# Performance work log

Hardware: AMD Instinct MI355X
Metric: run time of the kernel (lower is better)

The kernel has to match this reference:

```python
import jax, jax.numpy as jnp
import numpy as np

NUM_HEADS = 16

def setup_inputs() -> dict:
    key = jax.random.key(0)
    k1, k2, k3 = jax.random.split(key, 3)
    B, N, C = 2, 2048, 1024
    x = jax.random.normal(k1, (B, N, C), dtype=jnp.float32)
    w_qkv = jax.random.normal(k2, (C, 3 * C), dtype=jnp.float32) * (C ** -0.5)
    w_proj = jax.random.normal(k3, (C, C), dtype=jnp.float32) * (C ** -0.5)
    b_proj = jnp.zeros((C,), dtype=jnp.float32)
    return {"x": x, "w_qkv": w_qkv, "w_proj": w_proj, "b_proj": b_proj}

def reference(x, w_qkv, w_proj, b_proj):
    B, N, C = x.shape
    H = NUM_HEADS
    D = C // H
    scale = D ** -0.5
    qkv = (x @ w_qkv).reshape(B, N, 3, H, D).transpose(2, 0, 3, 1, 4)  # [3,B,H,N,D]
    q, k, v = qkv[0], qkv[1], qkv[2]
    attn = jnp.einsum("bhnd,bhmd->bhnm", q, k) * scale  # [B,H,N,N]
    attn = jax.nn.softmax(attn, axis=-1)
    out = jnp.einsum("bhnm,bhmd->bhnd", attn, v)  # [B,H,N,D]
    out = out.transpose(0, 2, 1, 3).reshape(B, N, C)
    return out @ w_proj + b_proj
```

## Files before the change

kernel.cpp:

```cpp
#include <hip/hip_runtime.h>
#include <hip/hip_bf16.h>
#include <math.h>

#define B_SZ   2
#define N_SEQ  2048
#define C_DIM  1024
#define H_NUM  16
#define D_HEAD 64
#define M_ROWS (B_SZ * N_SEQ)
#define QKV_N  (3 * C_DIM)

typedef __attribute__((ext_vector_type(8))) short  bf16x8;
typedef __attribute__((ext_vector_type(4))) float  floatx4;

static __device__ __forceinline__ unsigned short f2bf(float x) {
    unsigned int u = __float_as_uint(x);
    u = (u + 0x7FFFu + ((u >> 16) & 1u)) >> 16;
    return (unsigned short)u;
}
static __device__ __forceinline__ unsigned int f2bf_hi(float x) {
    unsigned int u = __float_as_uint(x);
    return u + 0x7FFFu + ((u >> 16) & 1u);
}
#if __has_builtin(__builtin_amdgcn_cvt_pk_bf16_f32)
typedef __bf16 bf16_2 __attribute__((ext_vector_type(2)));
static __device__ __forceinline__ unsigned int pkbf(float a, float b) {
    union { bf16_2 v; unsigned int u; } c;
    c.v = __builtin_amdgcn_cvt_pk_bf16_f32(a, b);
    return c.u;
}
#else
static __device__ __forceinline__ unsigned int pkbf(float a, float b) {
    return __builtin_amdgcn_perm(f2bf_hi(b), f2bf_hi(a), 0x07060302u);
}
#endif

#if __has_builtin(__builtin_amdgcn_exp2f)
#define EXP2F(x) __builtin_amdgcn_exp2f(x)
#else
#define EXP2F(x) exp2f(x)
#endif

#define GLP(p) ((const __attribute__((address_space(1))) void*)(p))
#define LDP(p) ((__attribute__((address_space(3))) void*)(p))

#define CEXP 0.18033688011112042f

__global__ __launch_bounds__(256)
void prep_fused(const float* __restrict__ x,      unsigned short* __restrict__ xb,
                const float* __restrict__ w_qkv,  unsigned short* __restrict__ wqkvT,
                const float* __restrict__ w_proj, unsigned short* __restrict__ wprojT)
{
    __shared__ unsigned short t[64][72];
    const int bid = blockIdx.x;
    const int tid = threadIdx.x;

    if (bid < 4096) {
        const int i = bid * 256 + tid;
        float4 v = ((const float4*)x)[i];
        ushort4 p;
        p.x = f2bf(v.x); p.y = f2bf(v.y); p.z = f2bf(v.z); p.w = f2bf(v.w);
        ((ushort4*)xb)[i] = p;
        return;
    }

    const float* W;
    unsigned short* WT;
    int N, tt;
    if (bid < 4096 + 768) { W = w_qkv;  WT = wqkvT;  N = QKV_N; tt = bid - 4096; }
    else                  { W = w_proj; WT = wprojT; N = C_DIM; tt = bid - 4864; }
    const int ntiles = N / 64;
    const int n0 = (tt % ntiles) * 64;
    const int k0 = (tt / ntiles) * 64;
    const int K  = C_DIM;

    const int tc = tid & 15;
    const int tr = tid >> 4;
    #pragma unroll
    for (int p = 0; p < 4; ++p) {
        const int r = tr + p * 16;
        float4 v = *(const float4*)&W[(size_t)(k0 + r) * N + n0 + tc * 4];
        ushort4 pk;
        pk.x = f2bf(v.x); pk.y = f2bf(v.y); pk.z = f2bf(v.z); pk.w = f2bf(v.w);
        *(ushort4*)&t[r][tc * 4] = pk;
    }
    __syncthreads();

    const int n  = tid >> 2;
    const int c0 = (tid & 3) * 16;
    unsigned short tmp[16];
    #pragma unroll
    for (int i = 0; i < 16; ++i) tmp[i] = t[c0 + i][n];
    *(uint4*)&WT[(size_t)(n0 + n) * K + k0 + c0]     = *(uint4*)&tmp[0];
    *(uint4*)&WT[(size_t)(n0 + n) * K + k0 + c0 + 8] = *(uint4*)&tmp[8];
}

__global__ __launch_bounds__(512, 2)
void gemm_qkv(const unsigned short* __restrict__ A,
              const unsigned short* __restrict__ BT,
              unsigned short* __restrict__ qbuf,
              unsigned short* __restrict__ kbuf,
              unsigned short* __restrict__ vbuf)
{
    extern __shared__ unsigned short lds2[];
    unsigned short* AsB = lds2;
    unsigned short* BsB = lds2 + 32768;

    const int K = C_DIM;
    const int tid  = threadIdx.x;
    const int lane = tid & 63;
    const int wave = tid >> 6;
    const int wm2  = wave >> 2;
    const int wn4  = wave & 3;
    const int l15  = lane & 15;
    const int lq   = lane >> 4;
    const int e7   = l15 & 7;

    const int bid = blockIdx.x;
    const int g   = (bid & 7) * 32 + (bid >> 3);
    const int bm  = (g & 15) * 256;
    const int bn  = (g >> 4) * 192;

    const int srow = tid >> 3;
    const int gso  = ((tid & 7) ^ (srow & 7)) * 8;

    const unsigned short* ga = A  + (size_t)(bm + srow) * K + gso;
    const unsigned short* gb = BT + (size_t)(bn + srow) * K + gso;

    floatx4 acc[8][3];
    #pragma unroll
    for (int i = 0; i < 8; ++i)
        #pragma unroll
        for (int j = 0; j < 3; ++j) acc[i][j] = (floatx4){0.f, 0.f, 0.f, 0.f};

#define QKV_STAGE(t_, buf_)                                                    \
    {                                                                          \
        unsigned short* Ad_ = AsB + (buf_) * 16384;                            \
        unsigned short* Bd_ = BsB + (buf_) * 12288;                            \
        _Pragma("unroll")                                                      \
        for (int i_ = 0; i_ < 4; ++i_)                                         \
            __builtin_amdgcn_global_load_lds(                                  \
                GLP(ga + (size_t)i_ * 64 * K + (t_) * 64),                     \
                LDP(Ad_ + i_ * 4096 + tid * 8), 16, 0, 0);                     \
        _Pragma("unroll")                                                      \
        for (int i_ = 0; i_ < 3; ++i_)                                         \
            __builtin_amdgcn_global_load_lds(                                  \
                GLP(gb + (size_t)i_ * 64 * K + (t_) * 64),                     \
                LDP(Bd_ + i_ * 4096 + tid * 8), 16, 0, 0);                     \
    }

    QKV_STAGE(0, 0);
    QKV_STAGE(1, 1);
    asm volatile("s_waitcnt vmcnt(7)\ns_barrier" ::: "memory");

    for (int t = 0; t < 16; ++t) {
        const int cur = t & 1;
        const unsigned short* Ac = AsB + cur * 16384;
        const unsigned short* Bc = BsB + cur * 12288;

        bf16x8 afl[2][4], bfr[2][3];
        #pragma unroll
        for (int kc = 0; kc < 2; ++kc) {
            #pragma unroll
            for (int mt = 0; mt < 4; ++mt)
                afl[kc][mt] = *(const bf16x8*)&Ac[(wm2 * 128 + mt * 16 + l15) * 64
                                                  + (((kc * 4 + lq) ^ e7) * 8)];
            #pragma unroll
            for (int nt = 0; nt < 3; ++nt)
                bfr[kc][nt] = *(const bf16x8*)&Bc[(wn4 * 48 + nt * 16 + l15) * 64
                                                  + (((kc * 4 + lq) ^ e7) * 8)];
        }

        __builtin_amdgcn_s_setprio(1);
        #pragma unroll
        for (int kc = 0; kc < 2; ++kc)
            #pragma unroll
            for (int mt = 0; mt < 4; ++mt)
                #pragma unroll
                for (int nt = 0; nt < 3; ++nt)
                    acc[mt][nt] = __builtin_amdgcn_mfma_f32_16x16x32_bf16(
                        afl[kc][mt], bfr[kc][nt], acc[mt][nt], 0, 0, 0);
        __builtin_amdgcn_s_setprio(0);

        bf16x8 afh[2][4];
        #pragma unroll
        for (int kc = 0; kc < 2; ++kc)
            #pragma unroll
            for (int mt = 0; mt < 4; ++mt)
                afh[kc][mt] = *(const bf16x8*)&Ac[(wm2 * 128 + 64 + mt * 16 + l15) * 64
                                                  + (((kc * 4 + lq) ^ e7) * 8)];

        asm volatile("s_waitcnt lgkmcnt(0)\ns_barrier" ::: "memory");

        if (t < 14) QKV_STAGE(t + 2, cur);

        __builtin_amdgcn_s_setprio(1);
        #pragma unroll
        for (int kc = 0; kc < 2; ++kc)
            #pragma unroll
            for (int mt = 0; mt < 4; ++mt)
                #pragma unroll
                for (int nt = 0; nt < 3; ++nt)
                    acc[4 + mt][nt] = __builtin_amdgcn_mfma_f32_16x16x32_bf16(
                        afh[kc][mt], bfr[kc][nt], acc[4 + mt][nt], 0, 0, 0);
        __builtin_amdgcn_s_setprio(0);

        if (t < 14)       asm volatile("s_waitcnt vmcnt(7)\ns_barrier" ::: "memory");
        else if (t == 14) asm volatile("s_waitcnt vmcnt(0)\ns_barrier" ::: "memory");
    }
#undef QKV_STAGE

    #pragma unroll
    for (int nt = 0; nt < 3; ++nt) {
        const int col  = bn + wn4 * 48 + nt * 16 + l15;
        const int reg3 = col >> 10;
        const int h    = (col >> 6) & 15;
        const int d    = col & 63;
        const float sc4 = (reg3 == 0) ? CEXP : 1.0f;
        #pragma unroll
        for (int mt = 0; mt < 8; ++mt) {
            const int row = bm + wm2 * 128 + mt * 16 + lq * 4;
            const int b   = row >> 11;
            const int n   = row & 2047;
            if (reg3 < 2) {
                unsigned short* dst = (reg3 ? kbuf : qbuf)
                    + ((size_t)(b * H_NUM + h) * N_SEQ + n) * D_HEAD + d;
                #pragma unroll
                for (int r = 0; r < 4; ++r)
                    dst[(size_t)r * D_HEAD] = f2bf(acc[mt][nt][r] * sc4);
            } else {
                const int a  = n & 63;
                const int fk = (a & 0x20) | ((a & 0x0C) << 1) | ((a & 0x10) >> 2);
                unsigned short* dst = vbuf
                    + ((size_t)(b * H_NUM + h) * D_HEAD + d) * N_SEQ + (n & ~63) + fk;
                ushort4 pk;
                pk.x = f2bf(acc[mt][nt][0]); pk.y = f2bf(acc[mt][nt][1]);
                pk.z = f2bf(acc[mt][nt][2]); pk.w = f2bf(acc[mt][nt][3]);
                *(ushort4*)dst = pk;
            }
        }
    }
}

__global__ __launch_bounds__(512, 4)
void attn_mfma(const unsigned short* __restrict__ qbuf,
               const unsigned short* __restrict__ kbuf,
               const unsigned short* __restrict__ vbuf,
               unsigned short* __restrict__ attnb)
{
    __shared__ unsigned short KsS[2][2][64 * 64];
    __shared__ unsigned short VtS[2][2][64 * 64];

    const int tid  = threadIdx.x;
    const int lane = tid & 63;
    const int wave = tid >> 6;
    const int grp  = wave >> 2;
    const int wrow = wave & 3;
    const int l15  = lane & 15;
    const int lq   = lane >> 4;
    const int e    = l15 & 7;

    const int bid  = blockIdx.x;
    const int bh   = (bid & 7) * 4 + (bid >> 7);
    const int qblk = (bid >> 3) & 15;
    const int b    = bh >> 4;
    const int h    = bh & 15;
    const int q0   = qblk * 128 + wrow * 32;

    const unsigned short* khead = kbuf + (size_t)bh * N_SEQ * D_HEAD;
    const unsigned short* vhead = vbuf + (size_t)bh * D_HEAD * N_SEQ;

    bf16x8 qf[2][2];
    #pragma unroll
    for (int qb = 0; qb < 2; ++qb) {
        const unsigned short* qrow = qbuf
            + ((size_t)bh * N_SEQ + q0 + qb * 16 + l15) * D_HEAD + lq * 8;
        qf[0][qb] = *(const bf16x8*)qrow;
        qf[1][qb] = *(const bf16x8*)(qrow + 32);
    }

    floatx4 acc[4][2];
    #pragma unroll
    for (int dc = 0; dc < 4; ++dc)
        #pragma unroll
        for (int qb = 0; qb < 2; ++qb) acc[dc][qb] = (floatx4){0.f, 0.f, 0.f, 0.f};
    float lsum[2] = {0.f, 0.f};

    const int srow = tid >> 3;
    const int gso  = ((tid & 7) ^ (srow & 7)) * 8;

    #pragma unroll
    for (int i = 0; i < 2; ++i) {
        __builtin_amdgcn_global_load_lds(GLP(khead + (size_t)(i * 64 + srow) * 64 + gso),
                                         LDP(&KsS[0][i][tid * 8]), 16, 0, 0);
        __builtin_amdgcn_global_load_lds(GLP(vhead + (size_t)srow * N_SEQ + i * 64 + gso),
                                         LDP(&VtS[0][i][tid * 8]), 16, 0, 0);
    }

    for (int s = 0; s < N_SEQ / 128; ++s) {
        const int cur = s & 1;
        __syncthreads();

        if (s + 1 < N_SEQ / 128) {
            const int m1 = (s + 1) * 128;
            const int nx = cur ^ 1;
            #pragma unroll
            for (int i = 0; i < 2; ++i) {
                __builtin_amdgcn_global_load_lds(
                    GLP(khead + (size_t)(m1 + i * 64 + srow) * 64 + gso),
                    LDP(&KsS[nx][i][tid * 8]), 16, 0, 0);
                __builtin_amdgcn_global_load_lds(
                    GLP(vhead + (size_t)srow * N_SEQ + m1 + i * 64 + gso),
                    LDP(&VtS[nx][i][tid * 8]), 16, 0, 0);
            }
        }

        const unsigned short* Ksc = &KsS[cur][grp][0];
        const unsigned short* Vtc = &VtS[cur][grp][0];

        floatx4 st[4][2];
        #pragma unroll
        for (int t = 0; t < 4; ++t) {
            bf16x8 k0 = *(const bf16x8*)&Ksc[(t * 16 + l15) * 64 + ((lq ^ e) * 8)];
            bf16x8 k1 = *(const bf16x8*)&Ksc[(t * 16 + l15) * 64 + (((4 + lq) ^ e) * 8)];
            #pragma unroll
            for (int qb = 0; qb < 2; ++qb) {
                floatx4 sv = (floatx4){-8.f, -8.f, -8.f, -8.f};
                sv = __builtin_amdgcn_mfma_f32_16x16x32_bf16(k0, qf[0][qb], sv, 0, 0, 0);
                sv = __builtin_amdgcn_mfma_f32_16x16x32_bf16(k1, qf[1][qb], sv, 0, 0, 0);
                st[t][qb] = sv;
            }
        }

        bf16x8 pf[2][2];
        #pragma unroll
        for (int qb = 0; qb < 2; ++qb) {
            unsigned int pk[8];
            float la = 0.f;
            #pragma unroll
            for (int t = 0; t < 4; ++t) {
                float p0 = EXP2F(st[t][qb][0]);
                float p1 = EXP2F(st[t][qb][1]);
                float p2 = EXP2F(st[t][qb][2]);
                float p3 = EXP2F(st[t][qb][3]);
                la += (p0 + p1) + (p2 + p3);
                pk[t * 2]     = pkbf(p0, p1);
                pk[t * 2 + 1] = pkbf(p2, p3);
            }
            lsum[qb] += la;
            union { uint4 u; bf16x8 v; } c0, c1;
            c0.u = make_uint4(pk[0], pk[1], pk[2], pk[3]);
            c1.u = make_uint4(pk[4], pk[5], pk[6], pk[7]);
            pf[0][qb] = c0.v;
            pf[1][qb] = c1.v;
        }

        #pragma unroll
        for (int dc = 0; dc < 4; ++dc) {
            bf16x8 v0 = *(const bf16x8*)&Vtc[(dc * 16 + l15) * 64 + ((lq ^ e) * 8)];
            bf16x8 v1 = *(const bf16x8*)&Vtc[(dc * 16 + l15) * 64 + (((4 + lq) ^ e) * 8)];
            #pragma unroll
            for (int qb = 0; qb < 2; ++qb) {
                acc[dc][qb] = __builtin_amdgcn_mfma_f32_16x16x32_bf16(
                    v0, pf[0][qb], acc[dc][qb], 0, 0, 0);
                acc[dc][qb] = __builtin_amdgcn_mfma_f32_16x16x32_bf16(
                    v1, pf[1][qb], acc[dc][qb], 0, 0, 0);
            }
        }
    }

    __syncthreads();
    float* smA = (float*)&KsS[0][0][0];
    float* smL = (float*)&VtS[0][0][0];
    const int li = wrow * 64 + lane;
    if (grp) {
        float* p = smA + li * 32;
        #pragma unroll
        for (int dc = 0; dc < 4; ++dc)
            #pragma unroll
            for (int qb = 0; qb < 2; ++qb)
                #pragma unroll
                for (int r = 0; r < 4; ++r)
                    p[(dc * 8 + qb * 4 + r) ^ (lane & 31)] = acc[dc][qb][r];
        smL[li * 2]     = lsum[0];
        smL[li * 2 + 1] = lsum[1];
    }
    __syncthreads();
    if (grp) return;

    {
        const float* p = smA + li * 32;
        #pragma unroll
        for (int dc = 0; dc < 4; ++dc)
            #pragma unroll
            for (int qb = 0; qb < 2; ++qb)
                #pragma unroll
                for (int r = 0; r < 4; ++r)
                    acc[dc][qb][r] += p[(dc * 8 + qb * 4 + r) ^ (lane & 31)];
        lsum[0] += smL[li * 2];
        lsum[1] += smL[li * 2 + 1];
    }

    #pragma unroll
    for (int qb = 0; qb < 2; ++qb) {
        float l = lsum[qb];
        l += __shfl_xor(l, 16, 64);
        l += __shfl_xor(l, 32, 64);
        const float inv = 1.f / l;
        const int q = q0 + qb * 16 + l15;
        unsigned short* orow = attnb + ((size_t)b * N_SEQ + q) * C_DIM + h * D_HEAD;
        #pragma unroll
        for (int dc = 0; dc < 4; ++dc) {
            ushort4 pkk;
            pkk.x = f2bf(acc[dc][qb][0] * inv);
            pkk.y = f2bf(acc[dc][qb][1] * inv);
            pkk.z = f2bf(acc[dc][qb][2] * inv);
            pkk.w = f2bf(acc[dc][qb][3] * inv);
            *(ushort4*)&orow[dc * 16 + lq * 4] = pkk;
        }
    }
}

__global__ __launch_bounds__(256)
void gemm_bt(const unsigned short* __restrict__ A,
             const unsigned short* __restrict__ BT,
             const float* __restrict__ bias,
             float* __restrict__ Cm,
             int M, int N, int K)
{
    __shared__ unsigned short As[128 * 64];
    __shared__ unsigned short Bs[64 * 64];

    const int tid  = threadIdx.x;
    const int lane = tid & 63;
    const int wave = tid >> 6;
    const int l15  = lane & 15;
    const int lq   = lane >> 4;
    const int e7   = l15 & 7;
    const int wm   = (wave & 1) * 64;
    const int wn   = (wave >> 1) * 32;

    const int bid = blockIdx.x;
    const int xcd = bid & 7;
    const int j   = bid >> 3;
    const int bm  = (j >> 1) * 128;
    const int bn  = ((j & 1) * 8 + xcd) * 64;

    const int srow = tid >> 3;
    const int gso  = ((tid & 7) ^ (srow & 7)) * 8;

    const unsigned short* ga = A  + (size_t)(bm + srow) * K + gso;
    const unsigned short* gb = BT + (size_t)(bn + srow) * K + gso;

    floatx4 acc[4][2];
    #pragma unroll
    for (int i = 0; i < 4; ++i)
        #pragma unroll
        for (int jj = 0; jj < 2; ++jj) acc[i][jj] = (floatx4){0.f, 0.f, 0.f, 0.f};

    for (int kt = 0; kt < K; kt += 64) {
        #pragma unroll
        for (int i = 0; i < 4; ++i)
            __builtin_amdgcn_global_load_lds(GLP(ga + (size_t)i * 32 * K + kt),
                                             LDP(&As[i * 2048 + tid * 8]), 16, 0, 0);
        #pragma unroll
        for (int i = 0; i < 2; ++i)
            __builtin_amdgcn_global_load_lds(GLP(gb + (size_t)i * 32 * K + kt),
                                             LDP(&Bs[i * 2048 + tid * 8]), 16, 0, 0);
        __syncthreads();

        bf16x8 af[2][4], bfr[2][2];
        #pragma unroll
        for (int t = 0; t < 4; ++t)
            #pragma unroll
            for (int kc = 0; kc < 2; ++kc)
                af[kc][t] = *(const bf16x8*)&As[(wm + t * 16 + l15) * 64
                                                + (((kc * 4 + lq) ^ e7) * 8)];
        #pragma unroll
        for (int t = 0; t < 2; ++t)
            #pragma unroll
            for (int kc = 0; kc < 2; ++kc)
                bfr[kc][t] = *(const bf16x8*)&Bs[(wn + t * 16 + l15) * 64
                                                 + (((kc * 4 + lq) ^ e7) * 8)];
        #pragma unroll
        for (int kc = 0; kc < 2; ++kc)
            #pragma unroll
            for (int mt = 0; mt < 4; ++mt)
                #pragma unroll
                for (int nt = 0; nt < 2; ++nt)
                    acc[mt][nt] = __builtin_amdgcn_mfma_f32_16x16x32_bf16(
                        af[kc][mt], bfr[kc][nt], acc[mt][nt], 0, 0, 0);
        __syncthreads();
    }

    float bv[2];
    #pragma unroll
    for (int nt = 0; nt < 2; ++nt) bv[nt] = bias[bn + wn + nt * 16 + l15];
    #pragma unroll
    for (int mt = 0; mt < 4; ++mt) {
        const int row = bm + wm + mt * 16 + lq * 4;
        #pragma unroll
        for (int nt = 0; nt < 2; ++nt) {
            const int col = bn + wn + nt * 16 + l15;
            #pragma unroll
            for (int r = 0; r < 4; ++r)
                Cm[(size_t)(row + r) * N + col] = acc[mt][nt][r] + bv[nt];
        }
    }
}

extern "C" void kernel_launch(void* const* d_in, const int* in_sizes, int n_in,
                              void* d_out, int out_size, void* d_ws, size_t ws_size,
                              hipStream_t stream)
{
    const float* x      = (const float*)d_in[0];
    const float* w_qkv  = (const float*)d_in[1];
    const float* w_proj = (const float*)d_in[2];
    const float* b_proj = (const float*)d_in[3];
    float*       out    = (float*)d_out;

    unsigned short* xb     = (unsigned short*)d_ws;
    unsigned short* wqkvT  = xb     + (size_t)M_ROWS * C_DIM;
    unsigned short* wprojT = wqkvT  + (size_t)QKV_N * C_DIM;
    unsigned short* qbuf   = wprojT + (size_t)C_DIM * C_DIM;
    unsigned short* kbuf   = qbuf   + (size_t)M_ROWS * C_DIM;
    unsigned short* vbuf   = kbuf   + (size_t)M_ROWS * C_DIM;
    unsigned short* attnb  = vbuf   + (size_t)M_ROWS * C_DIM;

    prep_fused<<<4096 + 768 + 256, 256, 0, stream>>>(x, xb, w_qkv, wqkvT, w_proj, wprojT);

    gemm_qkv<<<256, 512, 114688, stream>>>(xb, wqkvT, qbuf, kbuf, vbuf);

    attn_mfma<<<512, 512, 0, stream>>>(qbuf, kbuf, vbuf, attnb);

    gemm_bt<<<512, 256, 0, stream>>>(attnb, wprojT, b_proj, out, M_ROWS, C_DIM, C_DIM);
}
```

Before: 179.0 us.

## Double-buffer output projection GEMM with larger 256x64 tiles and split MFMA phases

The output projection GEMM now uses 512-thread blocks on 256x64 tiles with double-buffered LDS stages loaded asynchronously two steps ahead. MFMA work is split into two halves so the next stage's global-to-LDS loads are issued between them, with s_setprio raising the priority of the MFMA sections. The block-to-XCD mapping is changed to group M tiles per XCD. The aim is to hide global load latency and raise per-block reuse of the B tile, at the cost of 96KB of dynamic LDS and only 256 blocks.

```diff
diff --git a/kernel.cpp b/kernel.cpp
--- a/kernel.cpp
+++ b/kernel.cpp
@@ -421,30 +421,30 @@
     }
 }
 
-__global__ __launch_bounds__(256)
+__global__ __launch_bounds__(512, 2)
 void gemm_bt(const unsigned short* __restrict__ A,
              const unsigned short* __restrict__ BT,
              const float* __restrict__ bias,
              float* __restrict__ Cm,
              int M, int N, int K)
 {
-    __shared__ unsigned short As[128 * 64];
-    __shared__ unsigned short Bs[64 * 64];
+    extern __shared__ unsigned short ldsb[];
+    unsigned short* AsB = ldsb;
+    unsigned short* BsB = ldsb + 32768;
 
     const int tid  = threadIdx.x;
     const int lane = tid & 63;
     const int wave = tid >> 6;
+    const int wm2  = wave >> 2;
+    const int wn4  = wave & 3;
     const int l15  = lane & 15;
     const int lq   = lane >> 4;
     const int e7   = l15 & 7;
-    const int wm   = (wave & 1) * 64;
-    const int wn   = (wave >> 1) * 32;
 
     const int bid = blockIdx.x;
-    const int xcd = bid & 7;
-    const int j   = bid >> 3;
-    const int bm  = (j >> 1) * 128;
-    const int bn  = ((j & 1) * 8 + xcd) * 64;
+    const int g   = (bid & 7) * 32 + (bid >> 3);
+    const int bm  = (g & 15) * 256;
+    const int bn  = (g >> 4) * 64;
 
     const int srow = tid >> 3;
     const int gso  = ((tid & 7) ^ (srow & 7)) * 8;
@@ -452,60 +452,87 @@
     const unsigned short* ga = A  + (size_t)(bm + srow) * K + gso;
     const unsigned short* gb = BT + (size_t)(bn + srow) * K + gso;
 
-    floatx4 acc[4][2];
-    #pragma unroll
-    for (int i = 0; i < 4; ++i)
-        #pragma unroll
-        for (int jj = 0; jj < 2; ++jj) acc[i][jj] = (floatx4){0.f, 0.f, 0.f, 0.f};
-
-    for (int kt = 0; kt < K; kt += 64) {
-        #pragma unroll
-        for (int i = 0; i < 4; ++i)
-            __builtin_amdgcn_global_load_lds(GLP(ga + (size_t)i * 32 * K + kt),
-                                             LDP(&As[i * 2048 + tid * 8]), 16, 0, 0);
-        #pragma unroll
-        for (int i = 0; i < 2; ++i)
-            __builtin_amdgcn_global_load_lds(GLP(gb + (size_t)i * 32 * K + kt),
-                                             LDP(&Bs[i * 2048 + tid * 8]), 16, 0, 0);
-        __syncthreads();
-
-        bf16x8 af[2][4], bfr[2][2];
-        #pragma unroll
-        for (int t = 0; t < 4; ++t)
-            #pragma unroll
-            for (int kc = 0; kc < 2; ++kc)
-                af[kc][t] = *(const bf16x8*)&As[(wm + t * 16 + l15) * 64
-                                                + (((kc * 4 + lq) ^ e7) * 8)];
-        #pragma unroll
-        for (int t = 0; t < 2; ++t)
-            #pragma unroll
-            for (int kc = 0; kc < 2; ++kc)
-                bfr[kc][t] = *(const bf16x8*)&Bs[(wn + t * 16 + l15) * 64
-                                                 + (((kc * 4 + lq) ^ e7) * 8)];
+    floatx4 acc[8];
+    #pragma unroll
+    for (int i = 0; i < 8; ++i) acc[i] = (floatx4){0.f, 0.f, 0.f, 0.f};
+
+#define BT_STAGE(t_, buf_)                                                     \
+    {                                                                          \
+        unsigned short* Ad_ = AsB + (buf_) * 16384;                            \
+        unsigned short* Bd_ = BsB + (buf_) * 4096;                             \
+        _Pragma("unroll")                                                      \
+        for (int i_ = 0; i_ < 4; ++i_)                                         \
+            __builtin_amdgcn_global_load_lds(                                  \
+                GLP(ga + (size_t)i_ * 64 * K + (t_) * 64),                     \
+                LDP(Ad_ + i_ * 4096 + tid * 8), 16, 0, 0);                     \
+        __builtin_amdgcn_global_load_lds(                                      \
+            GLP(gb + (t_) * 64),                                               \
+            LDP(Bd_ + tid * 8), 16, 0, 0);                                     \
+    }
+
+    BT_STAGE(0, 0);
+    BT_STAGE(1, 1);
+    asm volatile("s_waitcnt vmcnt(5)\ns_barrier" ::: "memory");
+
+    for (int t = 0; t < 16; ++t) {
+        const int cur = t & 1;
+        const unsigned short* Ac = AsB + cur * 16384;
+        const unsigned short* Bc = BsB + cur * 4096;
+
+        bf16x8 afl[2][4], bfr[2];
+        #pragma unroll
+        for (int kc = 0; kc < 2; ++kc) {
+            #pragma unroll
+            for (int mt = 0; mt < 4; ++mt)
+                afl[kc][mt] = *(const bf16x8*)&Ac[(wm2 * 128 + mt * 16 + l15) * 64
+                                                  + (((kc * 4 + lq) ^ e7) * 8)];
+            bfr[kc] = *(const bf16x8*)&Bc[(wn4 * 16 + l15) * 64
+                                          + (((kc * 4 + lq) ^ e7) * 8)];
+        }
+
+        __builtin_amdgcn_s_setprio(1);
         #pragma unroll
         for (int kc = 0; kc < 2; ++kc)
             #pragma unroll
             for (int mt = 0; mt < 4; ++mt)
-                #pragma unroll
-                for (int nt = 0; nt < 2; ++nt)
-                    acc[mt][nt] = __builtin_amdgcn_mfma_f32_16x16x32_bf16(
-                        af[kc][mt], bfr[kc][nt], acc[mt][nt], 0, 0, 0);
-        __syncthreads();
-    }
-
-    float bv[2];
-    #pragma unroll
-    for (int nt = 0; nt < 2; ++nt) bv[nt] = bias[bn + wn + nt * 16 + l15];
-    #pragma unroll
-    for (int mt = 0; mt < 4; ++mt) {
-        const int row = bm + wm + mt * 16 + lq * 4;
-        #pragma unroll
-        for (int nt = 0; nt < 2; ++nt) {
-            const int col = bn + wn + nt * 16 + l15;
-            #pragma unroll
-            for (int r = 0; r < 4; ++r)
-                Cm[(size_t)(row + r) * N + col] = acc[mt][nt][r] + bv[nt];
-        }
+                acc[mt] = __builtin_amdgcn_mfma_f32_16x16x32_bf16(
+                    afl[kc][mt], bfr[kc], acc[mt], 0, 0, 0);
+        __builtin_amdgcn_s_setprio(0);
+
+        bf16x8 afh[2][4];
+        #pragma unroll
+        for (int kc = 0; kc < 2; ++kc)
+            #pragma unroll
+            for (int mt = 0; mt < 4; ++mt)
+                afh[kc][mt] = *(const bf16x8*)&Ac[(wm2 * 128 + 64 + mt * 16 + l15) * 64
+                                                  + (((kc * 4 + lq) ^ e7) * 8)];
+
+        asm volatile("s_waitcnt lgkmcnt(0)\ns_barrier" ::: "memory");
+
+        if (t < 14) BT_STAGE(t + 2, cur);
+
+        __builtin_amdgcn_s_setprio(1);
+        #pragma unroll
+        for (int kc = 0; kc < 2; ++kc)
+            #pragma unroll
+            for (int mt = 0; mt < 4; ++mt)
+                acc[4 + mt] = __builtin_amdgcn_mfma_f32_16x16x32_bf16(
+                    afh[kc][mt], bfr[kc], acc[4 + mt], 0, 0, 0);
+        __builtin_amdgcn_s_setprio(0);
+
+        if (t < 14)       asm volatile("s_waitcnt vmcnt(5)\ns_barrier" ::: "memory");
+        else if (t == 14) asm volatile("s_waitcnt vmcnt(0)\ns_barrier" ::: "memory");
+    }
+#undef BT_STAGE
+
+    const int col = bn + wn4 * 16 + l15;
+    const float bv = bias[col];
+    #pragma unroll
+    for (int mt = 0; mt < 8; ++mt) {
+        const int row = bm + wm2 * 128 + mt * 16 + lq * 4;
+        #pragma unroll
+        for (int r = 0; r < 4; ++r)
+            Cm[(size_t)(row + r) * N + col] = acc[mt][r] + bv;
     }
 }
 
@@ -533,5 +560,5 @@
 
     attn_mfma<<<512, 512, 0, stream>>>(qbuf, kbuf, vbuf, attnb);
 
-    gemm_bt<<<512, 256, 0, stream>>>(attnb, wprojT, b_proj, out, M_ROWS, C_DIM, C_DIM);
-}
+    gemm_bt<<<256, 512, 98304, stream>>>(attnb, wprojT, b_proj, out, M_ROWS, C_DIM, C_DIM);
+}
```

Result: no change. 178.0 us (-0.5%).
